# Kernel tuning notes

Measured on AMD Instinct MI355X. Metric: run time of the kernel, lower is better.

## Reference

```python
import jax, jax.numpy as jnp
import numpy as np

K_HEADS = 8
D_HEAD = 16
D_MODEL = K_HEADS * D_HEAD  # 128


def _xavier(key, shape):
    fan_in, fan_out = shape[0], shape[1]
    limit = (6.0 / (fan_in + fan_out)) ** 0.5
    return jax.random.uniform(key, shape, jnp.float32, -limit, limit)


def setup_inputs() -> dict:
    key = jax.random.key(0)
    ks = jax.random.split(key, 8)
    B, T, N = 8, 12, 512
    X = jax.random.normal(ks[0], (B, T, N, D_MODEL), jnp.float32)
    STE = jax.random.normal(ks[1], (B, T, N, 2 * D_MODEL), jnp.float32)
    Wq = _xavier(ks[2], (3 * D_MODEL, D_MODEL))
    Wk = _xavier(ks[3], (3 * D_MODEL, D_MODEL))
    Wv = _xavier(ks[4], (3 * D_MODEL, D_MODEL))
    Wo = _xavier(ks[5], (D_MODEL, D_MODEL))
    bq = jnp.zeros((D_MODEL,), jnp.float32)
    bk = jnp.zeros((D_MODEL,), jnp.float32)
    bv = jnp.zeros((D_MODEL,), jnp.float32)
    bo = jnp.zeros((D_MODEL,), jnp.float32)
    return {"X": X, "STE": STE, "Wq": Wq, "bq": bq, "Wk": Wk, "bk": bk,
            "Wv": Wv, "bv": bv, "Wo": Wo, "bo": bo}


def reference(X, STE, Wq, bq, Wk, bk, Wv, bv, Wo, bo):
    # 1x1-conv FCs == per-(t,node) linear + relu on the last dim
    H = jnp.concatenate([X, STE], axis=-1)              # [B,T,N,3D]
    q = jax.nn.relu(H @ Wq + bq)                        # [B,T,N,D]
    k = jax.nn.relu(H @ Wk + bk)
    v = jax.nn.relu(H @ Wv + bv)
    B, T, N, D = q.shape

    def heads(x):  # split last dim into K heads (head index major), move to front
        return x.reshape(B, T, N, K_HEADS, D_HEAD).transpose(3, 0, 1, 2, 4)

    qh, kh, vh = heads(q), heads(k), heads(v)           # [K,B,T,N,d]
    att = jnp.einsum('kbtnd,kbtmd->kbtnm', qh, kh) / (D_HEAD ** 0.5)
    att = jax.nn.softmax(att, axis=-1)                  # [K,B,T,N,N]
    o = jnp.einsum('kbtnm,kbtmd->kbtnd', att, vh)       # [K,B,T,N,d]
    o = o.transpose(1, 2, 3, 0, 4).reshape(B, T, N, D)  # concat heads on last dim
    return jax.nn.relu(o @ Wo + bo)
```

## Files before the change

kernel.cpp:

```cpp
#include <hip/hip_runtime.h>
#include <math.h>

constexpr int B_  = 8;
constexpr int T_  = 12;
constexpr int N_  = 512;
constexpr int DM  = 128;
constexpr int KH  = 8;
constexpr int DH  = 16;
constexpr int MR  = B_*T_*N_;
constexpr int K3  = 3*DM;
constexpr int TB  = 256;

typedef __attribute__((ext_vector_type(8))) short  bf16x8;
typedef __attribute__((ext_vector_type(4))) float  f32x4;
typedef __attribute__((ext_vector_type(4))) int    i32x4;

#define LOG2E 1.44269504088896340736f
#define SHIFT2 28.8539008177792681f

static __device__ inline float fast_exp2(float x) {
#if __has_builtin(__builtin_amdgcn_exp2f)
    return __builtin_amdgcn_exp2f(x);
#else
    return __expf(0.69314718055994531f * x);
#endif
}

static __device__ inline unsigned short f2bf(float x) {
    unsigned u = __float_as_uint(x);
    return (unsigned short)((u + 0x7fffu + ((u >> 16) & 1u)) >> 16);
}
static __device__ inline unsigned pk2(float a, float b) {
    unsigned ua = __float_as_uint(a) + 0x8000u;
    unsigned ub = __float_as_uint(b) + 0x8000u;
    return __builtin_amdgcn_perm(ub, ua, 0x07060302u);
}
static __device__ inline unsigned pk2t(float a, float b) {
    return __builtin_amdgcn_perm(__float_as_uint(b), __float_as_uint(a),
                                 0x07060302u);
}
static __device__ inline float fast_rcp(float x) {
#if __has_builtin(__builtin_amdgcn_rcpf)
    return __builtin_amdgcn_rcpf(x);
#else
    return 1.0f / x;
#endif
}

__global__ __launch_bounds__(256) void wprep_kernel(
    const float* __restrict__ Wq, const float* __restrict__ Wk,
    const float* __restrict__ Wv, const float* __restrict__ Wo,
    unsigned short* __restrict__ Wt, unsigned short* __restrict__ Wot)
{
    const int idx = blockIdx.x*256 + threadIdx.x;
    if (idx < 3*K3*DM) {
        const int p   = idx / (K3*DM);
        const int rem = idx - p*(K3*DM);
        const int k   = rem >> 7;
        const int n   = rem & 127;
        const float* W = (p == 0) ? Wq : ((p == 1) ? Wk : Wv);
        Wt[p*(K3*DM) + n*K3 + k] = f2bf(W[rem]);
    } else {
        const int i2 = idx - 3*K3*DM;
        const int k  = i2 >> 7;
        const int n  = i2 & 127;
        Wot[n*DM + k] = f2bf(Wo[i2]);
    }
}

__global__ __launch_bounds__(256, 2) void qkv_mfma(
    const float* __restrict__ X, const float* __restrict__ STE,
    const unsigned short* __restrict__ Wt,
    const float* __restrict__ bq, const float* __restrict__ bk,
    const float* __restrict__ bv,
    unsigned short* __restrict__ qb, unsigned short* __restrict__ kb2,
    unsigned short* __restrict__ vb2)
{
    __shared__ __align__(16) unsigned short Ash[128*72];
    __shared__ __align__(16) unsigned short Bsh[128*72];
    const int tid = threadIdx.x;
    const int rb  = blockIdx.x * 128;
    const int p   = blockIdx.y;
    const unsigned short* __restrict__ wtp = Wt + p*(K3*DM);
    const float* __restrict__ bias = (p == 0) ? bq : ((p == 1) ? bk : bv);
    unsigned short* __restrict__ outb = (p == 0) ? qb : ((p == 1) ? kb2 : vb2);
    const float scale = (p == 0) ? (0.25f * LOG2E) : 1.0f;

    const int lane = tid & 63, wv = tid >> 6;
    const int wm = (wv >> 1)*64, wn = (wv & 1)*64;
    const int m15 = lane & 15, g = lane >> 4;

    f32x4 acc[4][4] = {};

    for (int kt = 0; kt < K3; kt += 64) {
        const float* __restrict__ src = (kt < DM) ? (X + kt) : (STE + (kt - DM));
        const int ldr = (kt < DM) ? DM : 2*DM;
        #pragma unroll
        for (int i = 0; i < 8; ++i) {
            const int idx = tid + i*TB;
            const int m   = idx >> 4;
            const int c4  = idx & 15;
            const float4 f = *(const float4*)(src + (rb + m)*ldr + c4*4);
            uint2 d2;
            d2.x = pk2(f.x, f.y);
            d2.y = pk2(f.z, f.w);
            *(uint2*)(Ash + m*72 + c4*4) = d2;
        }
        #pragma unroll
        for (int i = 0; i < 4; ++i) {
            const int idx = tid + i*TB;
            const int n   = idx >> 3;
            const int kg  = idx & 7;
            *(uint4*)(Bsh + n*72 + kg*8) =
                *(const uint4*)(wtp + n*K3 + kt + kg*8);
        }
        __syncthreads();
        #pragma unroll
        for (int ks = 0; ks < 64; ks += 32) {
            bf16x8 af[4], bf[4];
            #pragma unroll
            for (int i = 0; i < 4; ++i)
                af[i] = *(const bf16x8*)(Ash + (wm + i*16 + m15)*72 + ks + g*8);
            #pragma unroll
            for (int j = 0; j < 4; ++j)
                bf[j] = *(const bf16x8*)(Bsh + (wn + j*16 + m15)*72 + ks + g*8);
            #pragma unroll
            for (int i = 0; i < 4; ++i)
                #pragma unroll
                for (int j = 0; j < 4; ++j)
                    acc[i][j] = __builtin_amdgcn_mfma_f32_16x16x32_bf16(
                        af[i], bf[j], acc[i][j], 0, 0, 0);
        }
        __syncthreads();
    }

    #pragma unroll
    for (int j = 0; j < 4; ++j) {
        const int c  = wn + j*16 + m15;
        const float bj = bias[c];
        const int h = c >> 4, d = c & 15;
        #pragma unroll
        for (int i = 0; i < 4; ++i) {
            #pragma unroll
            for (int r = 0; r < 4; ++r) {
                const int row = rb + wm + i*16 + g*4 + r;
                float v = acc[i][j][r] + bj;
                v = (v > 0.f ? v : 0.f) * scale;
                outb[(h*MR + row)*DH + d] = f2bf(v);
            }
        }
    }
}

__global__ __launch_bounds__(256, 3) void attn_kernel(
    const unsigned short* __restrict__ qb, const unsigned short* __restrict__ kb,
    const unsigned short* __restrict__ vb, unsigned short* __restrict__ ob)
{
    __shared__ __align__(16) unsigned short Klds[N_*DH];
    __shared__ __align__(16) unsigned short Vtlds[DH*536];

    const int tid = threadIdx.x;
    const int h   = blockIdx.x & (KH-1);
    const int bt  = blockIdx.x >> 3;
    const int base = (h*MR + bt*N_) * DH;

    {
        const uint4* kg = (const uint4*)(kb + base);
        uint4* kl = (uint4*)Klds;
        #pragma unroll
        for (int i = 0; i < 4; ++i) kl[tid + i*TB] = kg[tid + i*TB];
    }
    {
        const unsigned* vg = (const unsigned*)(vb + base);
        unsigned a[8], b[8];
        #pragma unroll
        for (int j = 0; j < 8; ++j) {
            a[j] = vg[(2*tid)*8 + j];
            b[j] = vg[(2*tid+1)*8 + j];
        }
        unsigned* vt = (unsigned*)Vtlds;
        #pragma unroll
        for (int d = 0; d < 16; ++d) {
            const int sh = (d & 1) * 16;
            const unsigned lo = (a[d >> 1] >> sh) & 0xffffu;
            const unsigned hi = (b[d >> 1] >> sh) & 0xffffu;
            vt[d*268 + tid] = lo | (hi << 16);
        }
    }
    __syncthreads();

    const int wv   = tid >> 6;
    const int lane = tid & 63;
    const int m    = lane & 15;
    const int g    = lane >> 4;

    bf16x8 qf[8];
    const unsigned short* qp = qb + base;
    #pragma unroll
    for (int j = 0; j < 8; ++j) {
        bf16x8 t = {0,0,0,0,0,0,0,0};
        if (g < 2) t = *(const bf16x8*)(qp + ((wv*8 + j)*16 + m)*DH + g*8);
        qf[j] = t;
    }

    const bf16x8 ones = {0x3F80,0x3F80,0x3F80,0x3F80,0x3F80,0x3F80,0x3F80,0x3F80};
    const f32x4 zshift = {-SHIFT2, -SHIFT2, -SHIFT2, -SHIFT2};

    f32x4 acc[8]  = {};
    f32x4 lacc[8] = {};

    for (int c = 0; c < 16; ++c) {
        const int kr0 = c*32 + ((m & 12) << 1) + (m & 3);
        bf16x8 kf0 = {0,0,0,0,0,0,0,0};
        bf16x8 kf1 = {0,0,0,0,0,0,0,0};
        if (g < 2) {
            kf0 = *(const bf16x8*)(Klds + kr0*DH + g*8);
            kf1 = *(const bf16x8*)(Klds + (kr0 + 4)*DH + g*8);
        }
        const bf16x8 vf = *(const bf16x8*)(Vtlds + m*536 + c*32 + g*8);

        #pragma unroll
        for (int j = 0; j < 8; ++j) {
            f32x4 s0 = __builtin_amdgcn_mfma_f32_16x16x32_bf16(kf0, qf[j], zshift, 0, 0, 0);
            f32x4 s1 = __builtin_amdgcn_mfma_f32_16x16x32_bf16(kf1, qf[j], zshift, 0, 0, 0);
            const float p0 = fast_exp2(s0[0]);
            const float p1 = fast_exp2(s0[1]);
            const float p2 = fast_exp2(s0[2]);
            const float p3 = fast_exp2(s0[3]);
            const float p4 = fast_exp2(s1[0]);
            const float p5 = fast_exp2(s1[1]);
            const float p6 = fast_exp2(s1[2]);
            const float p7 = fast_exp2(s1[3]);
            i32x4 pd = { (int)pk2t(p0, p1), (int)pk2t(p2, p3),
                         (int)pk2t(p4, p5), (int)pk2t(p6, p7) };
            const bf16x8 pf = __builtin_bit_cast(bf16x8, pd);
            acc[j]  = __builtin_amdgcn_mfma_f32_16x16x32_bf16(pf, vf,   acc[j],  0, 0, 0);
            lacc[j] = __builtin_amdgcn_mfma_f32_16x16x32_bf16(pf, ones, lacc[j], 0, 0, 0);
        }
    }

    #pragma unroll
    for (int j = 0; j < 8; ++j) {
        #pragma unroll
        for (int r = 0; r < 4; ++r) {
            const float iv = fast_rcp(lacc[j][r]);
            const int qrow = bt*N_ + (wv*8 + j)*16 + 4*g + r;
            ob[qrow*DM + h*DH + m] = f2bf(acc[j][r] * iv);
        }
    }
}

__global__ __launch_bounds__(256, 2) void out_mfma(
    const unsigned short* __restrict__ ot, const unsigned short* __restrict__ Wot,
    const float* __restrict__ bo, float* __restrict__ out)
{
    __shared__ __align__(16) unsigned short Ash[128*136];
    __shared__ __align__(16) unsigned short Bsh[128*136];
    const int tid = threadIdx.x;
    const int rb  = blockIdx.x * 128;
    const int lane = tid & 63, wv = tid >> 6;
    const int wm = (wv >> 1)*64, wn = (wv & 1)*64;
    const int m15 = lane & 15, g = lane >> 4;

    #pragma unroll
    for (int i = 0; i < 8; ++i) {
        const int idx = tid + i*TB;
        const int r  = idx >> 4;
        const int kg = idx & 15;
        *(uint4*)(Ash + r*136 + kg*8) = *(const uint4*)(ot + (rb + r)*DM + kg*8);
        *(uint4*)(Bsh + r*136 + kg*8) = *(const uint4*)(Wot + r*DM + kg*8);
    }
    __syncthreads();

    f32x4 acc[4][4] = {};
    #pragma unroll
    for (int ks = 0; ks < 128; ks += 32) {
        bf16x8 af[4], bf[4];
        #pragma unroll
        for (int i = 0; i < 4; ++i)
            af[i] = *(const bf16x8*)(Ash + (wm + i*16 + m15)*136 + ks + g*8);
        #pragma unroll
        for (int j = 0; j < 4; ++j)
            bf[j] = *(const bf16x8*)(Bsh + (wn + j*16 + m15)*136 + ks + g*8);
        #pragma unroll
        for (int i = 0; i < 4; ++i)
            #pragma unroll
            for (int j = 0; j < 4; ++j)
                acc[i][j] = __builtin_amdgcn_mfma_f32_16x16x32_bf16(
                    af[i], bf[j], acc[i][j], 0, 0, 0);
    }

    #pragma unroll
    for (int j = 0; j < 4; ++j) {
        const int c  = wn + j*16 + m15;
        const float bj = bo[c];
        #pragma unroll
        for (int i = 0; i < 4; ++i) {
            #pragma unroll
            for (int r = 0; r < 4; ++r) {
                const int row = rb + wm + i*16 + g*4 + r;
                float v = acc[i][j][r] + bj;
                out[row*DM + c] = v > 0.f ? v : 0.f;
            }
        }
    }
}

extern "C" void kernel_launch(void* const* d_in, const int* in_sizes, int n_in,
                              void* d_out, int out_size, void* d_ws, size_t ws_size,
                              hipStream_t stream)
{
    const float* X   = (const float*)d_in[0];
    const float* STE = (const float*)d_in[1];
    const float* Wq  = (const float*)d_in[2];
    const float* bq  = (const float*)d_in[3];
    const float* Wk  = (const float*)d_in[4];
    const float* bk  = (const float*)d_in[5];
    const float* Wv  = (const float*)d_in[6];
    const float* bv  = (const float*)d_in[7];
    const float* Wo  = (const float*)d_in[8];
    const float* bo  = (const float*)d_in[9];
    float* out = (float*)d_out;

    unsigned short* qb  = (unsigned short*)d_ws;
    unsigned short* kb  = qb  + (size_t)MR*DM;
    unsigned short* vb  = kb  + (size_t)MR*DM;
    unsigned short* ot  = vb  + (size_t)MR*DM;
    unsigned short* Wt  = ot  + (size_t)MR*DM;
    unsigned short* Wot = Wt  + (size_t)3*K3*DM;

    hipLaunchKernelGGL(wprep_kernel, dim3((3*K3*DM + DM*DM)/TB), dim3(TB), 0, stream,
                       Wq, Wk, Wv, Wo, Wt, Wot);
    hipLaunchKernelGGL(qkv_mfma, dim3(MR/128, 3), dim3(TB), 0, stream,
                       X, STE, Wt, bq, bk, bv, qb, kb, vb);
    hipLaunchKernelGGL(attn_kernel, dim3(KH*B_*T_), dim3(TB), 0, stream,
                       qb, kb, vb, ot);
    hipLaunchKernelGGL(out_mfma, dim3(MR/128), dim3(TB), 0, stream,
                       ot, Wot, bo, out);
}
```

Baseline: 190.7 us.

## Double-buffer QKV GEMM with register prefetch of next K-chunk

Loads of the next 64-wide K chunk of the activations and weights are issued into registers before the current chunk is converted and stored to LDS. LDS tiles are double-buffered so the trailing barrier per iteration can be dropped. The aim is to hide global-memory latency behind the MFMA work. In exchange, register use and LDS footprint rise sharply, which risks spills or lower occupancy.

```diff
diff --git a/kernel.cpp b/kernel.cpp
--- a/kernel.cpp
+++ b/kernel.cpp
@@ -76,8 +76,8 @@
     unsigned short* __restrict__ qb, unsigned short* __restrict__ kb2,
     unsigned short* __restrict__ vb2)
 {
-    __shared__ __align__(16) unsigned short Ash[128*72];
-    __shared__ __align__(16) unsigned short Bsh[128*72];
+    __shared__ __align__(16) unsigned short Ash[2][128*72];
+    __shared__ __align__(16) unsigned short Bsh[2][128*72];
     const int tid = threadIdx.x;
     const int rb  = blockIdx.x * 128;
     const int p   = blockIdx.y;
@@ -90,9 +90,16 @@
     const int wm = (wv >> 1)*64, wn = (wv & 1)*64;
     const int m15 = lane & 15, g = lane >> 4;
 
-    f32x4 acc[4][4] = {};
-
-    for (int kt = 0; kt < K3; kt += 64) {
+    const int am = tid >> 4;
+    const int ac4 = tid & 15;
+    const int bn  = tid >> 3;
+    const int bkg = tid & 7;
+
+    float4 areg[2][8];
+    uint4  breg[2][4];
+
+    auto issue = [&](int c, int s) {
+        const int kt = c*64;
         const float* __restrict__ src = (kt < DM) ? (X + kt) : (STE + (kt - DM));
         const int ldr = (kt < DM) ? DM : 2*DM;
         #pragma unroll
@@ -100,30 +107,55 @@
             const int idx = tid + i*TB;
             const int m   = idx >> 4;
             const int c4  = idx & 15;
-            const float4 f = *(const float4*)(src + (rb + m)*ldr + c4*4);
-            uint2 d2;
-            d2.x = pk2(f.x, f.y);
-            d2.y = pk2(f.z, f.w);
-            *(uint2*)(Ash + m*72 + c4*4) = d2;
+            areg[s][i] = *(const float4*)(src + (rb + m)*ldr + c4*4);
         }
         #pragma unroll
         for (int i = 0; i < 4; ++i) {
             const int idx = tid + i*TB;
             const int n   = idx >> 3;
             const int kg  = idx & 7;
-            *(uint4*)(Bsh + n*72 + kg*8) =
-                *(const uint4*)(wtp + n*K3 + kt + kg*8);
+            breg[s][i] = *(const uint4*)(wtp + n*K3 + kt + kg*8);
+        }
+    };
+
+    f32x4 acc[4][4] = {};
+
+    issue(0, 0);
+
+    #pragma unroll
+    for (int c = 0; c < K3/64; ++c) {
+        const int s = c & 1;
+        if (c + 1 < K3/64) issue(c + 1, s ^ 1);
+
+        #pragma unroll
+        for (int i = 0; i < 8; ++i) {
+            const int idx = tid + i*TB;
+            const int m   = idx >> 4;
+            const int c4  = idx & 15;
+            const float4 f = areg[s][i];
+            uint2 d2;
+            d2.x = pk2(f.x, f.y);
+            d2.y = pk2(f.z, f.w);
+            *(uint2*)(&Ash[s][m*72 + c4*4]) = d2;
+        }
+        #pragma unroll
+        for (int i = 0; i < 4; ++i) {
+            const int idx = tid + i*TB;
+            const int n   = idx >> 3;
+            const int kg  = idx & 7;
+            *(uint4*)(&Bsh[s][n*72 + kg*8]) = breg[s][i];
         }
         __syncthreads();
+
         #pragma unroll
         for (int ks = 0; ks < 64; ks += 32) {
             bf16x8 af[4], bf[4];
             #pragma unroll
             for (int i = 0; i < 4; ++i)
-                af[i] = *(const bf16x8*)(Ash + (wm + i*16 + m15)*72 + ks + g*8);
+                af[i] = *(const bf16x8*)(&Ash[s][(wm + i*16 + m15)*72 + ks + g*8]);
             #pragma unroll
             for (int j = 0; j < 4; ++j)
-                bf[j] = *(const bf16x8*)(Bsh + (wn + j*16 + m15)*72 + ks + g*8);
+                bf[j] = *(const bf16x8*)(&Bsh[s][(wn + j*16 + m15)*72 + ks + g*8]);
             #pragma unroll
             for (int i = 0; i < 4; ++i)
                 #pragma unroll
@@ -131,7 +163,6 @@
                     acc[i][j] = __builtin_amdgcn_mfma_f32_16x16x32_bf16(
                         af[i], bf[j], acc[i][j], 0, 0, 0);
         }
-        __syncthreads();
     }
 
     #pragma unroll
@@ -150,6 +181,7 @@
             }
         }
     }
+    (void)am; (void)ac4; (void)bn; (void)bkg;
 }
 
 __global__ __launch_bounds__(256, 3) void attn_kernel(
```

Measured after the change: 219.0 us. 1.15x slower.

## Load QKV GEMM tiles straight to LDS with XOR-swizzled layout

Applied to the files above, without the earlier changes.

The QKV projection kernel now uses global_load_lds (direct global-to-LDS DMA) for the fp32 activation and bf16 weight tiles, so the data no longer passes through registers. The fp32-to-bf16 conversion moves to the fragment read path, and the padded LDS layout is replaced with an XOR-swizzled one to avoid bank conflicts. The launch bounds now request 3 blocks per CU, which puts more pressure on registers. LDS per block grows because activations are stored as fp32, and every wave repeats the conversion work on each fragment read.

```diff
diff --git a/kernel.cpp b/kernel.cpp
--- a/kernel.cpp
+++ b/kernel.cpp
@@ -45,6 +45,12 @@
 #else
     return 1.0f / x;
 #endif
+}
+static __device__ inline void gl_lds16(const void* g, void* l) {
+    __builtin_amdgcn_global_load_lds(
+        (const __attribute__((address_space(1))) unsigned*)g,
+        (__attribute__((address_space(3))) unsigned*)l,
+        16, 0, 0);
 }
 
 __global__ __launch_bounds__(256) void wprep_kernel(
@@ -68,7 +74,7 @@
     }
 }
 
-__global__ __launch_bounds__(256, 2) void qkv_mfma(
+__global__ __launch_bounds__(256, 3) void qkv_mfma(
     const float* __restrict__ X, const float* __restrict__ STE,
     const unsigned short* __restrict__ Wt,
     const float* __restrict__ bq, const float* __restrict__ bk,
@@ -76,8 +82,8 @@
     unsigned short* __restrict__ qb, unsigned short* __restrict__ kb2,
     unsigned short* __restrict__ vb2)
 {
-    __shared__ __align__(16) unsigned short Ash[128*72];
-    __shared__ __align__(16) unsigned short Bsh[128*72];
+    __shared__ __align__(16) float          AshF[128*64];
+    __shared__ __align__(16) unsigned short Bsh[128*64];
     const int tid = threadIdx.x;
     const int rb  = blockIdx.x * 128;
     const int p   = blockIdx.y;
@@ -90,40 +96,52 @@
     const int wm = (wv >> 1)*64, wn = (wv & 1)*64;
     const int m15 = lane & 15, g = lane >> 4;
 
+    const int arl = lane >> 4, asl = lane & 15;
+    const int brl = lane >> 3, bsl = lane & 7;
+
     f32x4 acc[4][4] = {};
 
-    for (int kt = 0; kt < K3; kt += 64) {
+    for (int c = 0; c < K3/64; ++c) {
+        const int kt = c*64;
         const float* __restrict__ src = (kt < DM) ? (X + kt) : (STE + (kt - DM));
         const int ldr = (kt < DM) ? DM : 2*DM;
+
         #pragma unroll
         for (int i = 0; i < 8; ++i) {
-            const int idx = tid + i*TB;
-            const int m   = idx >> 4;
-            const int c4  = idx & 15;
-            const float4 f = *(const float4*)(src + (rb + m)*ldr + c4*4);
-            uint2 d2;
-            d2.x = pk2(f.x, f.y);
-            d2.y = pk2(f.z, f.w);
-            *(uint2*)(Ash + m*72 + c4*4) = d2;
+            const int rowbase = wv*32 + i*4;
+            const int row   = rowbase + arl;
+            const int chunk = asl ^ (row & 15);
+            gl_lds16(src + (rb + row)*ldr + chunk*4, &AshF[rowbase*64]);
         }
         #pragma unroll
         for (int i = 0; i < 4; ++i) {
-            const int idx = tid + i*TB;
-            const int n   = idx >> 3;
-            const int kg  = idx & 7;
-            *(uint4*)(Bsh + n*72 + kg*8) =
-                *(const uint4*)(wtp + n*K3 + kt + kg*8);
+            const int rowbase = wv*32 + i*8;
+            const int row   = rowbase + brl;
+            const int chunk = bsl ^ (row & 7);
+            gl_lds16(wtp + row*K3 + kt + chunk*8, &Bsh[rowbase*64]);
         }
         __syncthreads();
+
         #pragma unroll
         for (int ks = 0; ks < 64; ks += 32) {
             bf16x8 af[4], bf[4];
             #pragma unroll
-            for (int i = 0; i < 4; ++i)
-                af[i] = *(const bf16x8*)(Ash + (wm + i*16 + m15)*72 + ks + g*8);
-            #pragma unroll
-            for (int j = 0; j < 4; ++j)
-                bf[j] = *(const bf16x8*)(Bsh + (wn + j*16 + m15)*72 + ks + g*8);
+            for (int i = 0; i < 4; ++i) {
+                const int row = wm + i*16 + m15;
+                const int ch0 = (ks + g*8) >> 2;
+                const float4 lo = *(const float4*)&AshF[row*64 + ((ch0     ^ (row & 15)))*4];
+                const float4 hi = *(const float4*)&AshF[row*64 + (((ch0+1) ^ (row & 15)))*4];
+                uint4 d;
+                d.x = pk2(lo.x, lo.y); d.y = pk2(lo.z, lo.w);
+                d.z = pk2(hi.x, hi.y); d.w = pk2(hi.z, hi.w);
+                af[i] = __builtin_bit_cast(bf16x8, d);
+            }
+            #pragma unroll
+            for (int j = 0; j < 4; ++j) {
+                const int row = wn + j*16 + m15;
+                const int ch  = (ks >> 3) + g;
+                bf[j] = *(const bf16x8*)&Bsh[row*64 + (ch ^ (row & 7))*8];
+            }
             #pragma unroll
             for (int i = 0; i < 4; ++i)
                 #pragma unroll
```

Result: no change. 192.3 us (+0.8%).

## Load MFMA fragments directly from global memory in QKV and output GEMMs

Applied to the files above, without the earlier changes.

Removes the shared-memory staging and barriers from the QKV projection and output projection kernels. Each lane now loads its A and B MFMA fragments straight from global memory (converting fp32 inputs to bf16 in registers), and occupancy hints are raised from 2 to 3 blocks per CU. This cuts LDS traffic and synchronisation, but each row is fetched by two waves, so more redundant global and L2 loads go through the cache and the loads are less coalesced.

```diff
diff --git a/kernel.cpp b/kernel.cpp
--- a/kernel.cpp
+++ b/kernel.cpp
@@ -45,6 +45,14 @@
 #else
     return 1.0f / x;
 #endif
+}
+static __device__ inline bf16x8 afrag_f32(const float* p) {
+    const float4 lo = *(const float4*)(p);
+    const float4 hi = *(const float4*)(p + 4);
+    uint4 d;
+    d.x = pk2(lo.x, lo.y); d.y = pk2(lo.z, lo.w);
+    d.z = pk2(hi.x, hi.y); d.w = pk2(hi.z, hi.w);
+    return __builtin_bit_cast(bf16x8, d);
 }
 
 __global__ __launch_bounds__(256) void wprep_kernel(
@@ -68,7 +76,7 @@
     }
 }
 
-__global__ __launch_bounds__(256, 2) void qkv_mfma(
+__global__ __launch_bounds__(256, 3) void qkv_mfma(
     const float* __restrict__ X, const float* __restrict__ STE,
     const unsigned short* __restrict__ Wt,
     const float* __restrict__ bq, const float* __restrict__ bk,
@@ -76,8 +84,6 @@
     unsigned short* __restrict__ qb, unsigned short* __restrict__ kb2,
     unsigned short* __restrict__ vb2)
 {
-    __shared__ __align__(16) unsigned short Ash[128*72];
-    __shared__ __align__(16) unsigned short Bsh[128*72];
     const int tid = threadIdx.x;
     const int rb  = blockIdx.x * 128;
     const int p   = blockIdx.y;
@@ -90,48 +96,44 @@
     const int wm = (wv >> 1)*64, wn = (wv & 1)*64;
     const int m15 = lane & 15, g = lane >> 4;
 
+    const float* __restrict__ xrow[4];
+    const float* __restrict__ srow[4];
+    const unsigned short* __restrict__ wrow[4];
+    #pragma unroll
+    for (int i = 0; i < 4; ++i) {
+        const int arow = rb + wm + i*16 + m15;
+        xrow[i] = X   + (size_t)arow*DM     + g*8;
+        srow[i] = STE + (size_t)arow*(2*DM) + g*8;
+        wrow[i] = wtp + (wn + i*16 + m15)*K3 + g*8;
+    }
+
     f32x4 acc[4][4] = {};
 
-    for (int kt = 0; kt < K3; kt += 64) {
-        const float* __restrict__ src = (kt < DM) ? (X + kt) : (STE + (kt - DM));
-        const int ldr = (kt < DM) ? DM : 2*DM;
-        #pragma unroll
-        for (int i = 0; i < 8; ++i) {
-            const int idx = tid + i*TB;
-            const int m   = idx >> 4;
-            const int c4  = idx & 15;
-            const float4 f = *(const float4*)(src + (rb + m)*ldr + c4*4);
-            uint2 d2;
-            d2.x = pk2(f.x, f.y);
-            d2.y = pk2(f.z, f.w);
-            *(uint2*)(Ash + m*72 + c4*4) = d2;
-        }
-        #pragma unroll
-        for (int i = 0; i < 4; ++i) {
-            const int idx = tid + i*TB;
-            const int n   = idx >> 3;
-            const int kg  = idx & 7;
-            *(uint4*)(Bsh + n*72 + kg*8) =
-                *(const uint4*)(wtp + n*K3 + kt + kg*8);
-        }
-        __syncthreads();
-        #pragma unroll
-        for (int ks = 0; ks < 64; ks += 32) {
-            bf16x8 af[4], bf[4];
-            #pragma unroll
-            for (int i = 0; i < 4; ++i)
-                af[i] = *(const bf16x8*)(Ash + (wm + i*16 + m15)*72 + ks + g*8);
+    for (int kt = 0; kt < DM; kt += 32) {
+        bf16x8 af[4], bf[4];
+        #pragma unroll
+        for (int i = 0; i < 4; ++i) af[i] = afrag_f32(xrow[i] + kt);
+        #pragma unroll
+        for (int j = 0; j < 4; ++j) bf[j] = *(const bf16x8*)(wrow[j] + kt);
+        #pragma unroll
+        for (int i = 0; i < 4; ++i)
             #pragma unroll
             for (int j = 0; j < 4; ++j)
-                bf[j] = *(const bf16x8*)(Bsh + (wn + j*16 + m15)*72 + ks + g*8);
-            #pragma unroll
-            for (int i = 0; i < 4; ++i)
-                #pragma unroll
-                for (int j = 0; j < 4; ++j)
-                    acc[i][j] = __builtin_amdgcn_mfma_f32_16x16x32_bf16(
-                        af[i], bf[j], acc[i][j], 0, 0, 0);
-        }
-        __syncthreads();
+                acc[i][j] = __builtin_amdgcn_mfma_f32_16x16x32_bf16(
+                    af[i], bf[j], acc[i][j], 0, 0, 0);
+    }
+    for (int kt = 0; kt < 2*DM; kt += 32) {
+        bf16x8 af[4], bf[4];
+        #pragma unroll
+        for (int i = 0; i < 4; ++i) af[i] = afrag_f32(srow[i] + kt);
+        #pragma unroll
+        for (int j = 0; j < 4; ++j) bf[j] = *(const bf16x8*)(wrow[j] + DM + kt);
+        #pragma unroll
+        for (int i = 0; i < 4; ++i)
+            #pragma unroll
+            for (int j = 0; j < 4; ++j)
+                acc[i][j] = __builtin_amdgcn_mfma_f32_16x16x32_bf16(
+                    af[i], bf[j], acc[i][j], 0, 0, 0);
     }
 
     #pragma unroll
@@ -250,38 +252,32 @@
     }
 }
 
-__global__ __launch_bounds__(256, 2) void out_mfma(
+__global__ __launch_bounds__(256, 3) void out_mfma(
     const unsigned short* __restrict__ ot, const unsigned short* __restrict__ Wot,
     const float* __restrict__ bo, float* __restrict__ out)
 {
-    __shared__ __align__(16) unsigned short Ash[128*136];
-    __shared__ __align__(16) unsigned short Bsh[128*136];
     const int tid = threadIdx.x;
     const int rb  = blockIdx.x * 128;
     const int lane = tid & 63, wv = tid >> 6;
     const int wm = (wv >> 1)*64, wn = (wv & 1)*64;
     const int m15 = lane & 15, g = lane >> 4;
 
-    #pragma unroll
-    for (int i = 0; i < 8; ++i) {
-        const int idx = tid + i*TB;
-        const int r  = idx >> 4;
-        const int kg = idx & 15;
-        *(uint4*)(Ash + r*136 + kg*8) = *(const uint4*)(ot + (rb + r)*DM + kg*8);
-        *(uint4*)(Bsh + r*136 + kg*8) = *(const uint4*)(Wot + r*DM + kg*8);
-    }
-    __syncthreads();
+    const unsigned short* __restrict__ arow[4];
+    const unsigned short* __restrict__ brow[4];
+    #pragma unroll
+    for (int i = 0; i < 4; ++i) {
+        arow[i] = ot  + (size_t)(rb + wm + i*16 + m15)*DM + g*8;
+        brow[i] = Wot + (wn + i*16 + m15)*DM + g*8;
+    }
 
     f32x4 acc[4][4] = {};
     #pragma unroll
-    for (int ks = 0; ks < 128; ks += 32) {
+    for (int ks = 0; ks < DM; ks += 32) {
         bf16x8 af[4], bf[4];
         #pragma unroll
-        for (int i = 0; i < 4; ++i)
-            af[i] = *(const bf16x8*)(Ash + (wm + i*16 + m15)*136 + ks + g*8);
-        #pragma unroll
-        for (int j = 0; j < 4; ++j)
-            bf[j] = *(const bf16x8*)(Bsh + (wn + j*16 + m15)*136 + ks + g*8);
+        for (int i = 0; i < 4; ++i) af[i] = *(const bf16x8*)(arow[i] + ks);
+        #pragma unroll
+        for (int j = 0; j < 4; ++j) bf[j] = *(const bf16x8*)(brow[j] + ks);
         #pragma unroll
         for (int i = 0; i < 4; ++i)
             #pragma unroll
```

Measured after the change: 253.8 us. 1.33x slower.
